# Optimization experiments

Hardware: AMD Instinct MI355X
Metric: run time of the kernel (lower is better)

The kernel has to match this reference:

```python
import jax, jax.numpy as jnp
import numpy as np

B, S, HID, NH = 4, 1024, 1024, 16
DK = HID // NH
SCALE = DK ** -0.5
NEG = -9e15


def setup_inputs() -> dict:
    key = jax.random.key(0)
    ks = jax.random.split(key, 10)
    std = HID ** -0.5
    return {
        "batch": jax.random.normal(ks[0], (B, S, HID), jnp.float32),
        "attn_bias": jax.random.normal(ks[1], (B, NH, S, S), jnp.float32),
        "Wq": jax.random.normal(ks[2], (HID, HID), jnp.float32) * std,
        "bq": jnp.zeros((HID,), jnp.float32),
        "Wk": jax.random.normal(ks[3], (HID, HID), jnp.float32) * std,
        "bk": jnp.zeros((HID,), jnp.float32),
        "Wv": jax.random.normal(ks[4], (HID, HID), jnp.float32) * std,
        "bv": jnp.zeros((HID,), jnp.float32),
        "Wo": jax.random.normal(ks[5], (HID, HID), jnp.float32) * std,
        "bo": jnp.zeros((HID,), jnp.float32),
    }


def reference(batch, attn_bias, Wq, bq, Wk, bk, Wv, bv, Wo, bo):
    b, s, _ = batch.shape
    # QKV projections -> [b, h, s, d]
    q = (batch @ Wq.T + bq).reshape(b, s, NH, DK).transpose(0, 2, 1, 3)
    k = (batch @ Wk.T + bk).reshape(b, s, NH, DK).transpose(0, 2, 1, 3)
    v = (batch @ Wv.T + bv).reshape(b, s, NH, DK).transpose(0, 2, 1, 3)
    # scaled scores [b, h, s, s]
    x = jnp.einsum("bhqd,bhkd->bhqk", q * SCALE, k)
    # custom zero-mask: exact zeros become -9e15
    x = jnp.where(x == 0, jnp.float32(NEG), x)
    x = x + attn_bias
    p = jax.nn.softmax(x, axis=3)  # dropout_rate=0.0 -> identity
    o = jnp.einsum("bhqk,bhkd->bhqd", p, v)
    o = o.transpose(0, 2, 1, 3).reshape(b, s, NH * DK)
    return o @ Wo.T + bo
```

## Files before the change

### kernel.cpp

```cpp
#include <hip/hip_runtime.h>
#include <hip/hip_bf16.h>
#include <stdint.h>
#include <stddef.h>

#define Bd  4
#define Sd  1024
#define Hd  1024
#define NHd 16
#define DKd 64
#define SCALEF 0.125f
#define NEGV  -9.0e15f
#define L2E   1.4426950408889634f

typedef __attribute__((ext_vector_type(8))) short bfrag;
typedef __attribute__((ext_vector_type(4))) float facc;

typedef __attribute__((address_space(1))) const unsigned int ga_u32;
typedef __attribute__((address_space(3))) unsigned int ls_u32;

__device__ __forceinline__ void gload_lds16(const void* g, void* l) {
  __builtin_amdgcn_global_load_lds((ga_u32*)g, (ls_u32*)l, 16, 0, 0);
}

__device__ __forceinline__ unsigned short f2bf(float f) {
  unsigned int u = __float_as_uint(f);
  u += 0x7fffu + ((u >> 16) & 1u);
  return (unsigned short)(u >> 16);
}

__global__ void castk_all(const float* __restrict__ s0, const float* __restrict__ s1,
                          const float* __restrict__ s2, const float* __restrict__ s3,
                          const float* __restrict__ s4,
                          unsigned short* __restrict__ d0, unsigned short* __restrict__ d1,
                          unsigned short* __restrict__ d2, unsigned short* __restrict__ d3,
                          unsigned short* __restrict__ d4) {
  const int id = blockIdx.x;
  const float* s; unsigned short* d; int i;
  if (id < 4096) { s = s0; d = d0; i = id * 256 + threadIdx.x; }
  else {
    const int w = (id - 4096) >> 10;
    s = (w == 0) ? s1 : (w == 1) ? s2 : (w == 2) ? s3 : s4;
    d = (w == 0) ? d1 : (w == 1) ? d2 : (w == 2) ? d3 : d4;
    i = ((id - 4096) & 1023) * 256 + threadIdx.x;
  }
  float4 v = ((const float4*)s)[i];
  ushort4 ov;
  ov.x = f2bf(v.x); ov.y = f2bf(v.y); ov.z = f2bf(v.z); ov.w = f2bf(v.w);
  ((ushort4*)d)[i] = ov;
}

__global__ __launch_bounds__(256, 3)
void gemm_qkv(const unsigned short* __restrict__ A,
              const unsigned short* __restrict__ W0, const unsigned short* __restrict__ W1,
              const unsigned short* __restrict__ W2,
              const float* __restrict__ b0, const float* __restrict__ b1, const float* __restrict__ b2,
              unsigned short* __restrict__ o0, unsigned short* __restrict__ o1, unsigned short* __restrict__ o2) {
  __shared__ __align__(16) unsigned short smem[128 * 136];
  unsigned short* sA = smem;
  unsigned short* sB = smem + 4096;
  const int z = blockIdx.z;
  const unsigned short* Bm = (z == 0) ? W0 : (z == 1) ? W1 : W2;
  const float* bias = (z == 0) ? b0 : (z == 1) ? b1 : b2;
  unsigned short* out = (z == 0) ? o0 : (z == 1) ? o1 : o2;

  const int m0 = blockIdx.x * 128, n0 = blockIdx.y * 128;
  const int tid = threadIdx.x;
  const int wave = tid >> 6, lane = tid & 63;
  const int quad = lane >> 4, l16 = lane & 15;
  const int wm = wave >> 1, wn = wave & 1;

  facc acc[4][4] = {};

  const int j0 = wave * 128 + lane;
  const int j1 = j0 + 64;
  const int row0 = j0 >> 2, ko0 = (j0 & 3) << 3;
  const int row1 = j1 >> 2, ko1 = (j1 & 3) << 3;
  const size_t aoff0 = (size_t)(m0 + row0) * 1024 + ko0;
  const size_t aoff1 = (size_t)(m0 + row1) * 1024 + ko1;
  const size_t boff0 = (size_t)(n0 + row0) * 1024 + ko0;
  const size_t boff1 = (size_t)(n0 + row1) * 1024 + ko1;
  unsigned short* sA0 = sA + (wave * 2 + 0) * 512;
  unsigned short* sA1 = sA + (wave * 2 + 1) * 512;
  unsigned short* sB0 = sB + (wave * 2 + 0) * 512;
  unsigned short* sB1 = sB + (wave * 2 + 1) * 512;

  for (int k0 = 0; k0 < 1024; k0 += 32) {
    gload_lds16(A + aoff0 + k0, sA0);
    gload_lds16(A + aoff1 + k0, sA1);
    gload_lds16(Bm + boff0 + k0, sB0);
    gload_lds16(Bm + boff1 + k0, sB1);
    __syncthreads();
    bfrag af[4], bf[4];
#pragma unroll
    for (int i = 0; i < 4; ++i) af[i] = *(const bfrag*)(sA + (wm * 64 + i * 16 + l16) * 32 + quad * 8);
#pragma unroll
    for (int j = 0; j < 4; ++j) bf[j] = *(const bfrag*)(sB + (wn * 64 + j * 16 + l16) * 32 + quad * 8);
#pragma unroll
    for (int i = 0; i < 4; ++i)
#pragma unroll
      for (int j = 0; j < 4; ++j)
        acc[i][j] = __builtin_amdgcn_mfma_f32_16x16x32_bf16(af[i], bf[j], acc[i][j], 0, 0, 0);
    __syncthreads();
  }

  if (z < 2) {
#pragma unroll
    for (int i = 0; i < 4; ++i)
#pragma unroll
      for (int j = 0; j < 4; ++j) {
        const int col = n0 + wn * 64 + j * 16 + l16;
        const float bv = bias[col];
        const int h = col >> 6, d = col & 63;
#pragma unroll
        for (int r = 0; r < 4; ++r) {
          const int m = m0 + wm * 64 + i * 16 + quad * 4 + r;
          const int b = m >> 10, s = m & 1023;
          out[(((size_t)(b * NHd + h) * Sd) + s) * DKd + d] = f2bf(acc[i][j][r] + bv);
        }
      }
  } else {
    unsigned short* sT = smem;
#pragma unroll
    for (int i = 0; i < 4; ++i)
#pragma unroll
      for (int j = 0; j < 4; ++j) {
        const int col = n0 + wn * 64 + j * 16 + l16;
        const float bv = bias[col];
        const int nrow = wn * 64 + j * 16 + l16;
        const int mbase = wm * 64 + i * 16 + quad * 4;
        ushort4 pk;
        pk.x = f2bf(acc[i][j][0] + bv);
        pk.y = f2bf(acc[i][j][1] + bv);
        pk.z = f2bf(acc[i][j][2] + bv);
        pk.w = f2bf(acc[i][j][3] + bv);
        *(ushort4*)(sT + nrow * 136 + mbase) = pk;
      }
    __syncthreads();
    const int bI = m0 >> 10, s0i = m0 & 1023;
#pragma unroll
    for (int it = 0; it < 8; ++it) {
      const int c = tid + it * 256;
      const int row = c >> 4, mc = (c & 15) * 8;
      bfrag vv = *(const bfrag*)(sT + row * 136 + mc);
      const int col = n0 + row, hh = col >> 6, dd = col & 63;
      *(bfrag*)(out + (((size_t)(bI * NHd + hh) * DKd) + dd) * Sd + s0i + mc) = vv;
    }
  }
}

__global__ __launch_bounds__(256, 3)
void gemm_out(const unsigned short* __restrict__ A, const unsigned short* __restrict__ Bm,
              const float* __restrict__ bias, float* __restrict__ out) {
  __shared__ __align__(16) unsigned short sA[64 * 64];
  __shared__ __align__(16) unsigned short sB[128 * 64];
  const int m0 = blockIdx.x * 64, n0 = blockIdx.y * 128;
  const int tid = threadIdx.x;
  const int wave = tid >> 6, lane = tid & 63;
  const int quad = lane >> 4, l16 = lane & 15;

  facc acc[8] = {};

  const int cA0 = (wave * 2 + 0) * 64 + lane;
  const int cA1 = (wave * 2 + 1) * 64 + lane;
  const int rA0 = cA0 >> 3, kA0 = ((cA0 & 7) ^ (rA0 & 7)) * 8;
  const int rA1 = cA1 >> 3, kA1 = ((cA1 & 7) ^ (rA1 & 7)) * 8;
  const size_t aoff0 = (size_t)(m0 + rA0) * 1024 + kA0;
  const size_t aoff1 = (size_t)(m0 + rA1) * 1024 + kA1;
  size_t boff[4];
#pragma unroll
  for (int i = 0; i < 4; ++i) {
    const int c = (wave * 4 + i) * 64 + lane;
    const int r = c >> 3, kk = ((c & 7) ^ (r & 7)) * 8;
    boff[i] = (size_t)(n0 + r) * 1024 + kk;
  }

  for (int k0 = 0; k0 < 1024; k0 += 64) {
    gload_lds16(A + aoff0 + k0, sA + (wave * 2 + 0) * 512);
    gload_lds16(A + aoff1 + k0, sA + (wave * 2 + 1) * 512);
#pragma unroll
    for (int i = 0; i < 4; ++i)
      gload_lds16(Bm + boff[i] + k0, sB + (wave * 4 + i) * 512);
    __syncthreads();
#pragma unroll
    for (int c2 = 0; c2 < 2; ++c2) {
      const int ko = ((c2 * 4 + quad) ^ (l16 & 7)) * 8;
      bfrag af = *(const bfrag*)(sA + (wave * 16 + l16) * 64 + ko);
#pragma unroll
      for (int j = 0; j < 8; ++j) {
        bfrag bf = *(const bfrag*)(sB + (j * 16 + l16) * 64 + ko);
        acc[j] = __builtin_amdgcn_mfma_f32_16x16x32_bf16(af, bf, acc[j], 0, 0, 0);
      }
    }
    __syncthreads();
  }

#pragma unroll
  for (int j = 0; j < 8; ++j) {
    const int col = n0 + j * 16 + l16;
    const float bv = bias[col];
#pragma unroll
    for (int r = 0; r < 4; ++r) {
      const int m = m0 + wave * 16 + quad * 4 + r;
      out[(size_t)m * 1024 + col] = acc[j][r] + bv;
    }
  }
}

__global__ __launch_bounds__(128, 4)
void attn_kernel(const unsigned short* __restrict__ q,
                 const unsigned short* __restrict__ k,
                 const unsigned short* __restrict__ vt,
                 const float* __restrict__ bias,
                 unsigned short* __restrict__ o)
{
  __shared__ __align__(16) unsigned short sP[2 * 16 * 136];
  const int bh = blockIdx.y;
  const int q0 = blockIdx.x * 32;
  const int tid = threadIdx.x;
  const int wave = tid >> 6, lane = tid & 63;
  const int quad = lane >> 4, l16 = lane & 15;
  const int b = bh >> 4, h = bh & 15;

  const unsigned short* qh = q + (size_t)bh * Sd * DKd;
  const unsigned short* kh = k + (size_t)bh * Sd * DKd;
  const unsigned short* vh = vt + (size_t)bh * DKd * Sd;
  const float* bias_h = bias + (size_t)bh * Sd * Sd;
  const int rq = q0 + wave * 16;
  unsigned short* sPw = sP + wave * 16 * 136;

  bfrag qf[2];
#pragma unroll
  for (int c = 0; c < 2; ++c)
    qf[c] = *(const bfrag*)(qh + (size_t)(rq + l16) * DKd + c * 32 + quad * 8);

  facc oacc[4] = {};
  float lsum[4] = {0.f, 0.f, 0.f, 0.f};
  const float SL2 = SCALEF * L2E;

  float br[4][8];
  const float* bp0 = bias_h + (size_t)(rq + quad * 4) * Sd + l16;
#pragma unroll
  for (int r = 0; r < 4; ++r)
#pragma unroll
    for (int j = 0; j < 8; ++j)
      br[r][j] = bp0[r * Sd + j * 16];

  for (int t = 0; t < 8; ++t) {
    const int k0 = t * 128;
    facc sacc[8] = {};
#pragma unroll
    for (int c = 0; c < 2; ++c)
#pragma unroll
      for (int j = 0; j < 8; ++j) {
        bfrag kf = *(const bfrag*)(kh + (size_t)(k0 + j * 16 + l16) * DKd + c * 32 + quad * 8);
        sacc[j] = __builtin_amdgcn_mfma_f32_16x16x32_bf16(qf[c], kf, sacc[j], 0, 0, 0);
      }
#pragma unroll
    for (int r = 0; r < 4; ++r)
#pragma unroll
      for (int j = 0; j < 8; ++j) {
        const float x = sacc[j][r];
        float e = exp2f(fmaf(x, SL2, br[r][j] * L2E));
        e = (x == 0.0f) ? 0.0f : e;
        sacc[j][r] = e;
        lsum[r] += e;
      }
    if (t < 7) {
      const float* bp = bp0 + k0 + 128;
#pragma unroll
      for (int r = 0; r < 4; ++r)
#pragma unroll
        for (int j = 0; j < 8; ++j)
          br[r][j] = bp[r * Sd + j * 16];
    }
#pragma unroll
    for (int j = 0; j < 8; ++j)
#pragma unroll
      for (int r = 0; r < 4; ++r)
        sPw[(quad * 4 + r) * 136 + j * 16 + l16] = f2bf(sacc[j][r]);
#pragma unroll
    for (int c = 0; c < 4; ++c) {
      bfrag pf = *(const bfrag*)(sPw + l16 * 136 + c * 32 + quad * 8);
#pragma unroll
      for (int n = 0; n < 4; ++n) {
        bfrag vf = *(const bfrag*)(vh + (size_t)(n * 16 + l16) * Sd + k0 + c * 32 + quad * 8);
        oacc[n] = __builtin_amdgcn_mfma_f32_16x16x32_bf16(pf, vf, oacc[n], 0, 0, 0);
      }
    }
  }

#pragma unroll
  for (int r = 0; r < 4; ++r) {
#pragma unroll
    for (int s = 1; s < 16; s <<= 1) lsum[r] += __shfl_xor(lsum[r], s, 64);
  }
#pragma unroll
  for (int r = 0; r < 4; ++r) {
    const float rinv = 1.0f / lsum[r];
    const size_t rowo = (size_t)(b * Sd + rq + quad * 4 + r) * Hd + h * 64;
#pragma unroll
    for (int n = 0; n < 4; ++n)
      o[rowo + n * 16 + l16] = f2bf(oacc[n][r] * rinv);
  }
}

extern "C" void kernel_launch(void* const* d_in, const int* in_sizes, int n_in,
                              void* d_out, int out_size, void* d_ws, size_t ws_size,
                              hipStream_t stream) {
  const float* batch = (const float*)d_in[0];
  const float* attn_bias = (const float*)d_in[1];
  const float* Wq = (const float*)d_in[2];
  const float* bq = (const float*)d_in[3];
  const float* Wk = (const float*)d_in[4];
  const float* bk = (const float*)d_in[5];
  const float* Wv = (const float*)d_in[6];
  const float* bv = (const float*)d_in[7];
  const float* Wo = (const float*)d_in[8];
  const float* bo = (const float*)d_in[9];
  float* out = (float*)d_out;

  unsigned short* ws = (unsigned short*)d_ws;
  unsigned short* Ab  = ws;
  unsigned short* Wqb = Ab  + 4194304;
  unsigned short* Wkb = Wqb + 1048576;
  unsigned short* Wvb = Wkb + 1048576;
  unsigned short* Wob = Wvb + 1048576;
  unsigned short* qb  = Wob + 1048576;
  unsigned short* kb  = qb  + 4194304;
  unsigned short* vtb = kb  + 4194304;
  unsigned short* ob  = vtb + 4194304;

  castk_all<<<8192, 256, 0, stream>>>(batch, Wq, Wk, Wv, Wo, Ab, Wqb, Wkb, Wvb, Wob);
  gemm_qkv<<<dim3(32, 8, 3), 256, 0, stream>>>(Ab, Wqb, Wkb, Wvb, bq, bk, bv, qb, kb, vtb);
  attn_kernel<<<dim3(32, 64), 128, 0, stream>>>(qb, kb, vtb, attn_bias, ob);
  gemm_out<<<dim3(64, 8), 256, 0, stream>>>(ob, Wob, bo, out);
}
```

Before: 542.7 us.

## Split attention key range across two waves with LDS reduction of partial outputs

Each attention block now handles 16 query rows instead of 32, and its two waves each process half of the key range (512 keys), reducing the partial O accumulators and row sums through shared memory. This doubles the grid to 4096 blocks and shrinks per-wave register and LDS use, aiming for more parallelism and occupancy in the bias-streaming attention kernel. The cost is that each block reloads K/V for fewer query rows, so K/V traffic doubles, and there is an extra LDS reduction and sync. The GEMM launch bounds are also lowered from 3 to 2 blocks per CU, and the attention kernel's is raised to 6.

Result: slower. 589.0 us (+8.5%).

```diff
diff --git a/kernel.cpp b/kernel.cpp
--- a/kernel.cpp
+++ b/kernel.cpp
@@ -49,7 +49,7 @@
   ((ushort4*)d)[i] = ov;
 }
 
-__global__ __launch_bounds__(256, 3)
+__global__ __launch_bounds__(256, 2)
 void gemm_qkv(const unsigned short* __restrict__ A,
               const unsigned short* __restrict__ W0, const unsigned short* __restrict__ W1,
               const unsigned short* __restrict__ W2,
@@ -148,7 +148,7 @@
   }
 }
 
-__global__ __launch_bounds__(256, 3)
+__global__ __launch_bounds__(256, 2)
 void gemm_out(const unsigned short* __restrict__ A, const unsigned short* __restrict__ Bm,
               const float* __restrict__ bias, float* __restrict__ out) {
   __shared__ __align__(16) unsigned short sA[64 * 64];
@@ -206,16 +206,17 @@
   }
 }
 
-__global__ __launch_bounds__(128, 4)
+__global__ __launch_bounds__(128, 6)
 void attn_kernel(const unsigned short* __restrict__ q,
                  const unsigned short* __restrict__ k,
                  const unsigned short* __restrict__ vt,
                  const float* __restrict__ bias,
                  unsigned short* __restrict__ o)
 {
-  __shared__ __align__(16) unsigned short sP[2 * 16 * 136];
+  __shared__ __align__(16) unsigned short sP[2 * 16 * 72];
+  __shared__ __align__(16) float sRed[64 * 20];
   const int bh = blockIdx.y;
-  const int q0 = blockIdx.x * 32;
+  const int q0 = blockIdx.x * 16;
   const int tid = threadIdx.x;
   const int wave = tid >> 6, lane = tid & 63;
   const int quad = lane >> 4, l16 = lane & 15;
@@ -225,82 +226,101 @@
   const unsigned short* kh = k + (size_t)bh * Sd * DKd;
   const unsigned short* vh = vt + (size_t)bh * DKd * Sd;
   const float* bias_h = bias + (size_t)bh * Sd * Sd;
-  const int rq = q0 + wave * 16;
-  unsigned short* sPw = sP + wave * 16 * 136;
+  unsigned short* sPw = sP + wave * 16 * 72;
+  const int cbase = wave * 512;
 
   bfrag qf[2];
 #pragma unroll
   for (int c = 0; c < 2; ++c)
-    qf[c] = *(const bfrag*)(qh + (size_t)(rq + l16) * DKd + c * 32 + quad * 8);
+    qf[c] = *(const bfrag*)(qh + (size_t)(q0 + l16) * DKd + c * 32 + quad * 8);
 
   facc oacc[4] = {};
   float lsum[4] = {0.f, 0.f, 0.f, 0.f};
   const float SL2 = SCALEF * L2E;
 
-  float br[4][8];
-  const float* bp0 = bias_h + (size_t)(rq + quad * 4) * Sd + l16;
+  float br[4][4];
+  const float* bp0 = bias_h + (size_t)(q0 + quad * 4) * Sd + cbase + l16;
 #pragma unroll
   for (int r = 0; r < 4; ++r)
 #pragma unroll
-    for (int j = 0; j < 8; ++j)
+    for (int j = 0; j < 4; ++j)
       br[r][j] = bp0[r * Sd + j * 16];
 
-  for (int t = 0; t < 8; ++t) {
-    const int k0 = t * 128;
-    facc sacc[8] = {};
+  for (int u = 0; u < 8; ++u) {
+    const int c0 = cbase + u * 64;
+    facc sacc[4] = {};
 #pragma unroll
     for (int c = 0; c < 2; ++c)
 #pragma unroll
-      for (int j = 0; j < 8; ++j) {
-        bfrag kf = *(const bfrag*)(kh + (size_t)(k0 + j * 16 + l16) * DKd + c * 32 + quad * 8);
+      for (int j = 0; j < 4; ++j) {
+        bfrag kf = *(const bfrag*)(kh + (size_t)(c0 + j * 16 + l16) * DKd + c * 32 + quad * 8);
         sacc[j] = __builtin_amdgcn_mfma_f32_16x16x32_bf16(qf[c], kf, sacc[j], 0, 0, 0);
       }
 #pragma unroll
     for (int r = 0; r < 4; ++r)
 #pragma unroll
-      for (int j = 0; j < 8; ++j) {
+      for (int j = 0; j < 4; ++j) {
         const float x = sacc[j][r];
         float e = exp2f(fmaf(x, SL2, br[r][j] * L2E));
         e = (x == 0.0f) ? 0.0f : e;
         sacc[j][r] = e;
         lsum[r] += e;
       }
-    if (t < 7) {
-      const float* bp = bp0 + k0 + 128;
+    if (u < 7) {
+      const float* bp = bp0 + (u + 1) * 64;
 #pragma unroll
       for (int r = 0; r < 4; ++r)
 #pragma unroll
-        for (int j = 0; j < 8; ++j)
+        for (int j = 0; j < 4; ++j)
           br[r][j] = bp[r * Sd + j * 16];
     }
 #pragma unroll
-    for (int j = 0; j < 8; ++j)
+    for (int j = 0; j < 4; ++j)
 #pragma unroll
       for (int r = 0; r < 4; ++r)
-        sPw[(quad * 4 + r) * 136 + j * 16 + l16] = f2bf(sacc[j][r]);
-#pragma unroll
-    for (int c = 0; c < 4; ++c) {
-      bfrag pf = *(const bfrag*)(sPw + l16 * 136 + c * 32 + quad * 8);
+        sPw[(quad * 4 + r) * 72 + j * 16 + l16] = f2bf(sacc[j][r]);
+#pragma unroll
+    for (int c2 = 0; c2 < 2; ++c2) {
+      bfrag pf = *(const bfrag*)(sPw + l16 * 72 + c2 * 32 + quad * 8);
 #pragma unroll
       for (int n = 0; n < 4; ++n) {
-        bfrag vf = *(const bfrag*)(vh + (size_t)(n * 16 + l16) * Sd + k0 + c * 32 + quad * 8);
+        bfrag vf = *(const bfrag*)(vh + (size_t)(n * 16 + l16) * Sd + c0 + c2 * 32 + quad * 8);
         oacc[n] = __builtin_amdgcn_mfma_f32_16x16x32_bf16(pf, vf, oacc[n], 0, 0, 0);
       }
     }
   }
 
-#pragma unroll
-  for (int r = 0; r < 4; ++r) {
-#pragma unroll
-    for (int s = 1; s < 16; s <<= 1) lsum[r] += __shfl_xor(lsum[r], s, 64);
-  }
-#pragma unroll
-  for (int r = 0; r < 4; ++r) {
-    const float rinv = 1.0f / lsum[r];
-    const size_t rowo = (size_t)(b * Sd + rq + quad * 4 + r) * Hd + h * 64;
+  if (wave == 1) {
 #pragma unroll
     for (int n = 0; n < 4; ++n)
-      o[rowo + n * 16 + l16] = f2bf(oacc[n][r] * rinv);
+#pragma unroll
+      for (int r = 0; r < 4; ++r)
+        sRed[lane * 20 + n * 4 + r] = oacc[n][r];
+#pragma unroll
+    for (int r = 0; r < 4; ++r) sRed[lane * 20 + 16 + r] = lsum[r];
+  }
+  __syncthreads();
+  if (wave == 0) {
+#pragma unroll
+    for (int n = 0; n < 4; ++n)
+#pragma unroll
+      for (int r = 0; r < 4; ++r)
+        oacc[n][r] += sRed[lane * 20 + n * 4 + r];
+#pragma unroll
+    for (int r = 0; r < 4; ++r) lsum[r] += sRed[lane * 20 + 16 + r];
+#pragma unroll
+    for (int r = 0; r < 4; ++r) {
+#pragma unroll
+      for (int s = 1; s < 16; s <<= 1) lsum[r] += __shfl_xor(lsum[r], s, 64);
+    }
+#pragma unroll
+    for (int r = 0; r < 4; ++r) {
+      const float rinv = 1.0f / lsum[r];
+      const size_t rowo = (size_t)(b * Sd + q0 + quad * 4 + r) * Hd + h * 64;
+#pragma unroll
+      for (int n = 0; n < 4; ++n)
+        o[rowo + n * 16 + l16] = f2bf(oacc[n][r] * rinv);
+    }
   }
 }
 
@@ -332,6 +352,6 @@
 
   castk_all<<<8192, 256, 0, stream>>>(batch, Wq, Wk, Wv, Wo, Ab, Wqb, Wkb, Wvb, Wob);
   gemm_qkv<<<dim3(32, 8, 3), 256, 0, stream>>>(Ab, Wqb, Wkb, Wvb, bq, bk, bv, qb, kb, vtb);
-  attn_kernel<<<dim3(32, 64), 128, 0, stream>>>(qb, kb, vtb, attn_bias, ob);
+  attn_kernel<<<dim3(64, 64), 128, 0, stream>>>(qb, kb, vtb, attn_bias, ob);
   gemm_out<<<dim3(64, 8), 256, 0, stream>>>(ob, Wob, bo, out);
 }
```
